# Kernel tuning notes

Hardware: AMD Instinct MI355X
Metric: run time of the kernel (lower is better)

## Reference

```python
import jax, jax.numpy as jnp
import numpy as np

EPS = 1e-5  # torch BatchNorm2d default


def _conv5x5(x, w, b):
    # x: [N,1,H,W], w: [1,1,5,5], b: [1]; stride 1, padding 2 (SAME)
    out = jax.lax.conv_general_dilated(
        x, w, window_strides=(1, 1), padding=((2, 2), (2, 2)),
        dimension_numbers=("NCHW", "OIHW", "NCHW"))
    return out + b[None, :, None, None]


def _batchnorm(x, gamma, beta):
    # training-mode BatchNorm2d: per-channel batch stats over (N,H,W), biased var
    mean = jnp.mean(x, axis=(0, 2, 3), keepdims=True)
    var = jnp.mean(jnp.square(x - mean), axis=(0, 2, 3), keepdims=True)
    xhat = (x - mean) * jax.lax.rsqrt(var + EPS)
    return xhat * gamma[None, :, None, None] + beta[None, :, None, None]


def _shrinkage(x, lumdb):
    return x + 0.5 * (jnp.sqrt(jnp.square(x - lumdb) + 1.0)
                      - jnp.sqrt(jnp.square(x + lumdb) + 1.0))


def setup_inputs() -> dict:
    key = jax.random.key(0)
    k1, k2, k3 = jax.random.split(key, 3)
    y = jax.random.normal(k1, (64, 1, 512, 512), dtype=jnp.float32)
    # kaiming-uniform-ish init for a 1x1x5x5 conv
    fan_in = 25.0
    bound = 1.0 / np.sqrt(fan_in)
    conv_w = jax.random.uniform(k2, (1, 1, 5, 5), jnp.float32, -bound, bound)
    conv_b = jax.random.uniform(k3, (1,), jnp.float32, -bound, bound)
    gamma = jnp.ones((1,), jnp.float32)
    beta = jnp.zeros((1,), jnp.float32)
    lambd = jnp.array([2.0, 1.0, 0.0], jnp.float32)
    return {"y": y, "conv_w": conv_w, "conv_b": conv_b,
            "gamma": gamma, "beta": beta, "lambd": lambd}


def reference(y, conv_w, conv_b, gamma, beta, lambd):
    x_k = y
    # unrolled LISTA iteration 1
    x = _batchnorm(_conv5x5(x_k, conv_w, conv_b), gamma, beta)
    x = _shrinkage(x, lambd[0])
    o12 = _batchnorm(_conv5x5(x, conv_w, conv_b), gamma, beta)
    x = _batchnorm(_conv5x5(x_k, conv_w, conv_b), gamma, beta)
    # iteration 2
    x = _shrinkage(o12 + x, lambd[1])
    o22 = _batchnorm(_conv5x5(x, conv_w, conv_b), gamma, beta)
    x = _batchnorm(_conv5x5(x_k, conv_w, conv_b), gamma, beta)
    # iteration 3
    x = _shrinkage(o22 + x, lambd[2])
    return x
```

## Files before the change

kernel.cpp:

```cpp
#include <hip/hip_runtime.h>
#include <math.h>

#define HH 512
#define WW 512
#define NTOT (64u*512u*512u)
#define TS 128
#define TROWS 132
#define TCH 18
#define TPIT 152
#define NTASK (TROWS*TCH)
#define NITER 10
#define NPART 4096

typedef __attribute__((ext_vector_type(8))) short short8;
typedef __attribute__((ext_vector_type(4))) float f32x4;

__device__ __forceinline__ float fsqrtf(float x) { return __builtin_amdgcn_sqrtf(x); }

__device__ __forceinline__ float shrinkf(float x, float l) {
    float a = x - l, b = x + l;
    return x + 0.5f * (fsqrtf(__builtin_fmaf(a, a, 1.f)) - fsqrtf(__builtin_fmaf(b, b, 1.f)));
}

__device__ __forceinline__ float bf2f(unsigned int u) {
    union { unsigned int i; float f; } cv; cv.i = u << 16; return cv.f;
}
__device__ __forceinline__ float lo2f(unsigned int p) {
    union { unsigned int i; float f; } cv; cv.i = p << 16; return cv.f;
}
__device__ __forceinline__ float hi2f(unsigned int p) {
    union { unsigned int i; float f; } cv; cv.i = p & 0xffff0000u; return cv.f;
}

__device__ __forceinline__ unsigned int cvtpk(float lo, float hi) {
    unsigned int r;
    asm("v_cvt_pk_bf16_f32 %0, %1, %2" : "=v"(r) : "v"(lo), "v"(hi));
    return r;
}

__device__ __forceinline__ void bf8(uint4 u, float* f) {
    f[0] = bf2f(u.x & 0xffffu); f[1] = bf2f(u.x >> 16);
    f[2] = bf2f(u.y & 0xffffu); f[3] = bf2f(u.y >> 16);
    f[4] = bf2f(u.z & 0xffffu); f[5] = bf2f(u.z >> 16);
    f[6] = bf2f(u.w & 0xffffu); f[7] = bf2f(u.w >> 16);
}

__device__ __forceinline__ void stats_fast(
    const float* __restrict__ part, double* __restrict__ sbuf,
    int tid, int lane, int wv,
    float gam, float bet, float& scl_out, float& shf_out)
{
    double sd = 0.0, qd = 0.0;
#pragma unroll
    for (int k = 0; k < 16; k++) {
        const int i = tid + k * 256;
        sd += (double)part[2 * i];
        qd += (double)part[2 * i + 1];
    }
#pragma unroll
    for (int off = 32; off > 0; off >>= 1) {
        sd += __shfl_xor(sd, off);
        qd += __shfl_xor(qd, off);
    }
    if (lane == 0) { sbuf[2 * wv] = sd; sbuf[2 * wv + 1] = qd; }
    __syncthreads();
    const double S = sbuf[0] + sbuf[2] + sbuf[4] + sbuf[6];
    const double Q = sbuf[1] + sbuf[3] + sbuf[5] + sbuf[7];
    const double mean = S / (double)NTOT;
    const double var  = Q / (double)NTOT - mean * mean;
    const double scl  = (double)gam / sqrt(var + 1e-5);
    scl_out = (float)scl;
    shf_out = (float)((double)bet - mean * scl);
}

template <int MODE, bool OBF>
__global__ __launch_bounds__(256, 4) void conv_k(
    const float* __restrict__ yin,
    const unsigned short* __restrict__ t1,
    const unsigned short* __restrict__ t2,
    unsigned short* __restrict__ outbf,
    float* __restrict__ outf32,
    const float* __restrict__ wgt,
    const float* __restrict__ bias,
    const float* __restrict__ prevPart,
    const float* __restrict__ statsIn,
    float* __restrict__ statsOut,
    const float* __restrict__ gamma,
    const float* __restrict__ beta,
    const float* __restrict__ lambd,
    float* __restrict__ partials)
{
    __shared__ unsigned short tile[TROWS * TPIT];
    __shared__ double sbuf[8];

    const int tid = threadIdx.x;
    const int lin = blockIdx.x;
    const int swz = ((lin & 7) << 7) | (lin >> 3);
    const int img = swz >> 4;
    const int rem = swz & 15;
    const int by = ((rem >> 2) & 3) * TS;
    const int bx = (rem & 3) * TS;
    const size_t ibase = (size_t)img * (HH * WW);

    const int lane = tid & 63;
    const int lm = lane & 15;
    const int kb = lane >> 4;
    const int wv = tid >> 6;

    float wloc[25];
#pragma unroll
    for (int i = 0; i < 25; i++) wloc[i] = wgt[i];
    const int basei = kb * 8 - lm - 6;
    short8 bfr[5];
#pragma unroll
    for (int ky = 0; ky < 5; ky++) {
        unsigned pkw[4];
#pragma unroll
        for (int jj = 0; jj < 4; jj++) {
            float v0 = 0.f, v1 = 0.f;
            const int i0 = basei + 2 * jj, i1 = i0 + 1;
#pragma unroll
            for (int t = 0; t < 5; t++) {
                if (i0 == t) v0 = wloc[ky * 5 + t];
                if (i1 == t) v1 = wloc[ky * 5 + t];
            }
            pkw[jj] = cvtpk(v0, v1);
        }
        union { unsigned u[4]; short8 s; } cv;
        cv.u[0]=pkw[0]; cv.u[1]=pkw[1]; cv.u[2]=pkw[2]; cv.u[3]=pkw[3];
        bfr[ky] = cv.s;
    }

    auto loadT = [&](int task, uint4& A, uint4& B) {
        A = make_uint4(0u,0u,0u,0u); B = make_uint4(0u,0u,0u,0u);
        const int row = task / TCH;
        const int ch  = task - row * TCH;
        const int gy  = by + row - 2;
        const int gx0 = bx + ch * 8 - 8;
        if (task < NTASK && gy >= 0 && gy < HH && gx0 >= 0 && gx0 <= WW - 8) {
            const size_t g = ibase + (size_t)gy * WW + gx0;
            if constexpr (MODE == 0) {
                A = *(const uint4*)(yin + g);
                B = *(const uint4*)(yin + g + 4);
            } else if constexpr (MODE == 1) {
                A = *(const uint4*)(t1 + g);
            } else {
                A = *(const uint4*)(t1 + g);
                B = *(const uint4*)(t2 + g);
            }
        }
    };

    uint4 sA0, sB0, sA1, sB1, sA2, sB2;
    loadT(tid,        sA0, sB0);
    loadT(tid + 256,  sA1, sB1);
    loadT(tid + 512,  sA2, sB2);

    float s1 = 0.f, h1 = 0.f, s2v = 0.f, h2 = 0.f, lam = 0.f;
    if constexpr (MODE == 1) {
        stats_fast(prevPart, sbuf, tid, lane, wv, gamma[0], beta[0], s1, h1);
        lam = lambd[0];
        if (lin == 0 && tid == 0) { statsOut[0] = s1; statsOut[1] = h1; }
    }
    if constexpr (MODE == 2) {
        stats_fast(prevPart, sbuf, tid, lane, wv, gamma[0], beta[0], s2v, h2);
        s1 = statsIn[0]; h1 = statsIn[1];
        lam = lambd[1];
    }

    auto procT = [&](int task, uint4 A, uint4 B) {
        const int row = task / TCH;
        const int ch  = task - row * TCH;
        uint4 pk = make_uint4(0u,0u,0u,0u);
        if constexpr (MODE == 0) {
            const float4 a = *(const float4*)&A;
            const float4 b = *(const float4*)&B;
            pk.x = cvtpk(a.x, a.y); pk.y = cvtpk(a.z, a.w);
            pk.z = cvtpk(b.x, b.y); pk.w = cvtpk(b.z, b.w);
        } else if constexpr (MODE == 1) {
            float f1[8]; bf8(A, f1);
            float v[8];
#pragma unroll
            for (int k = 0; k < 8; k++)
                v[k] = shrinkf(__builtin_fmaf(f1[k], s1, h1), lam);
            pk.x = cvtpk(v[0], v[1]); pk.y = cvtpk(v[2], v[3]);
            pk.z = cvtpk(v[4], v[5]); pk.w = cvtpk(v[6], v[7]);
        } else {
            float f1[8], f2[8]; bf8(A, f1); bf8(B, f2);
            float v[8];
#pragma unroll
            for (int k = 0; k < 8; k++) {
                float x = __builtin_fmaf(f2[k], s2v, h2)
                        + __builtin_fmaf(f1[k], s1, h1);
                v[k] = shrinkf(x, lam);
            }
            pk.x = cvtpk(v[0], v[1]); pk.y = cvtpk(v[2], v[3]);
            pk.z = cvtpk(v[4], v[5]); pk.w = cvtpk(v[6], v[7]);
        }
        const int gy  = by + row - 2;
        const int gx0 = bx + ch * 8 - 8;
        if (!(gy >= 0 && gy < HH && gx0 >= 0 && gx0 <= WW - 8))
            pk = make_uint4(0u,0u,0u,0u);
        *(uint4*)&tile[row * TPIT + ch * 8] = pk;
    };

#pragma unroll
    for (int t = 0; t < NITER; t++) {
        const int task = tid + t * 256;
        if (task < NTASK) procT(task, sA0, sB0);
        sA0 = sA1; sB0 = sB1;
        sA1 = sA2; sB1 = sB2;
        if (t + 3 < NITER) loadT(tid + (t + 3) * 256, sA2, sB2);
        else { sA2 = make_uint4(0u,0u,0u,0u); sB2 = make_uint4(0u,0u,0u,0u); }
    }

    const float b0 = bias[0];
    __syncthreads();

    const int r0w = wv * 32;

    f32x4 acc[2][8];
#pragma unroll
    for (int st = 0; st < 2; st++)
#pragma unroll
        for (int ct = 0; ct < 8; ct++)
            acc[st][ct] = (f32x4){0.f, 0.f, 0.f, 0.f};

#pragma unroll
    for (int ky = 0; ky < 5; ky++) {
        const short8 b = bfr[ky];
#pragma unroll
        for (int st = 0; st < 2; st++) {
            const unsigned short* ab = &tile[(r0w + st * 16 + lm + ky) * TPIT + kb * 8];
#pragma unroll
            for (int ct = 0; ct < 8; ct++) {
                short8 a = *(const short8*)(ab + ct * 16);
                acc[st][ct] = __builtin_amdgcn_mfma_f32_16x16x32_bf16(a, b, acc[st][ct], 0, 0, 0);
            }
        }
    }

    float s = 0.f, q = 0.f;
#pragma unroll
    for (int st = 0; st < 2; st++) {
#pragma unroll
        for (int ct = 0; ct < 8; ct++) {
            const f32x4 a = acc[st][ct];
            const int grow0 = by + r0w + st * 16 + kb * 4;
            const size_t base = ibase + (size_t)grow0 * WW + bx + ct * 16 + lm;
            if constexpr (OBF) {
                unsigned p01 = cvtpk(a[0] + b0, a[1] + b0);
                unsigned p23 = cvtpk(a[2] + b0, a[3] + b0);
                outbf[base]          = (unsigned short)(p01 & 0xffffu);
                outbf[base + WW]     = (unsigned short)(p01 >> 16);
                outbf[base + 2 * WW] = (unsigned short)(p23 & 0xffffu);
                outbf[base + 3 * WW] = (unsigned short)(p23 >> 16);
                float fr0 = lo2f(p01), fr1 = hi2f(p01), fr2 = lo2f(p23), fr3 = hi2f(p23);
                s += fr0 + fr1 + fr2 + fr3;
                q = __builtin_fmaf(fr0, fr0, __builtin_fmaf(fr1, fr1,
                    __builtin_fmaf(fr2, fr2, __builtin_fmaf(fr3, fr3, q))));
            } else {
                float f0 = a[0] + b0, f1v = a[1] + b0, f2v = a[2] + b0, f3v = a[3] + b0;
                outf32[base]          = f0;
                outf32[base + WW]     = f1v;
                outf32[base + 2 * WW] = f2v;
                outf32[base + 3 * WW] = f3v;
                s += f0 + f1v + f2v + f3v;
                q = __builtin_fmaf(f0, f0, __builtin_fmaf(f1v, f1v,
                    __builtin_fmaf(f2v, f2v, __builtin_fmaf(f3v, f3v, q))));
            }
        }
    }

#pragma unroll
    for (int off = 32; off > 0; off >>= 1) {
        s += __shfl_xor(s, off);
        q += __shfl_xor(q, off);
    }
    if (lane == 0) {
        partials[(swz * 4 + wv) * 2]     = s;
        partials[(swz * 4 + wv) * 2 + 1] = q;
    }
}

template <bool T3BF>
__global__ __launch_bounds__(256) void final_k(
    const unsigned short* __restrict__ t1,
    const unsigned short* __restrict__ t3b,
    float* __restrict__ io,
    const float* __restrict__ p3,
    const float* __restrict__ statsIn,
    const float* __restrict__ gamma,
    const float* __restrict__ beta,
    const float* __restrict__ lambd)
{
    __shared__ double sbuf[8];
    const int tid = threadIdx.x;
    const int lane = tid & 63;
    const int wv = tid >> 6;

    float s3, h3;
    stats_fast(p3, sbuf, tid, lane, wv, gamma[0], beta[0], s3, h3);
    const float s1 = statsIn[0], h1 = statsIn[1];
    const float lam = lambd[2];

#pragma unroll
    for (int c = 0; c < 8; c++) {
        const size_t idx = ((size_t)c * 1024 + blockIdx.x) * 256 + tid;
        const size_t base = idx * 8;

        uint4 u1 = *(const uint4*)(t1 + base);
        float f1[8]; bf8(u1, f1);

        float t3v[8];
        if constexpr (T3BF) {
            uint4 u3 = *(const uint4*)(t3b + base);
            bf8(u3, t3v);
        } else {
            float4 a0 = *(const float4*)(io + base);
            float4 a1 = *(const float4*)(io + base + 4);
            t3v[0]=a0.x; t3v[1]=a0.y; t3v[2]=a0.z; t3v[3]=a0.w;
            t3v[4]=a1.x; t3v[5]=a1.y; t3v[6]=a1.z; t3v[7]=a1.w;
        }

        float r[8];
#pragma unroll
        for (int k = 0; k < 8; k++) {
            float v = __builtin_fmaf(t3v[k], s3, h3) + __builtin_fmaf(f1[k], s1, h1);
            r[k] = shrinkf(v, lam);
        }
        *(float4*)(io + base)     = make_float4(r[0], r[1], r[2], r[3]);
        *(float4*)(io + base + 4) = make_float4(r[4], r[5], r[6], r[7]);
    }
}

extern "C" void kernel_launch(void* const* d_in, const int* in_sizes, int n_in,
                              void* d_out, int out_size, void* d_ws, size_t ws_size,
                              hipStream_t stream)
{
    const float* y     = (const float*)d_in[0];
    const float* wgt   = (const float*)d_in[1];
    const float* bias  = (const float*)d_in[2];
    const float* gamma = (const float*)d_in[3];
    const float* beta  = (const float*)d_in[4];
    const float* lambd = (const float*)d_in[5];
    float* out = (float*)d_out;

    char* ws = (char*)d_ws;
    unsigned short* t1 = (unsigned short*)ws;
    unsigned short* t2 = (unsigned short*)(ws + 33554432ull);
    unsigned short* t3 = (unsigned short*)(ws + 67108864ull);
    const bool t3bf = (ws_size >= 100761608ull);
    const size_t poff = t3bf ? 100663296ull : 67108864ull;
    float* p1    = (float*)(ws + poff);
    float* p2    = (float*)(ws + poff + 32768ull);
    float* p3    = (float*)(ws + poff + 65536ull);
    float* stats = (float*)(ws + poff + 98304ull);

    dim3 grid(1024, 1, 1), blk(256, 1, 1);
    conv_k<0, true><<<grid, blk, 0, stream>>>(y, nullptr, nullptr, t1, nullptr,
                                              wgt, bias, nullptr, nullptr, nullptr,
                                              gamma, beta, lambd, p1);
    conv_k<1, true><<<grid, blk, 0, stream>>>(nullptr, t1, nullptr, t2, nullptr,
                                              wgt, bias, p1, nullptr, stats,
                                              gamma, beta, lambd, p2);
    if (t3bf) {
        conv_k<2, true><<<grid, blk, 0, stream>>>(nullptr, t1, t2, t3, nullptr,
                                                  wgt, bias, p2, stats, nullptr,
                                                  gamma, beta, lambd, p3);
        final_k<true><<<grid, blk, 0, stream>>>(t1, t3, out, p3, stats,
                                                gamma, beta, lambd);
    } else {
        conv_k<2, false><<<grid, blk, 0, stream>>>(nullptr, t1, t2, nullptr, out,
                                                   wgt, bias, p2, stats, nullptr,
                                                   gamma, beta, lambd, p3);
        final_k<false><<<grid, blk, 0, stream>>>(t1, nullptr, out, p3, stats,
                                                 gamma, beta, lambd);
    }
}
```

Baseline: 91.30 us.

## Process two tiles per block with async global-to-LDS loads overlapping MFMA

Splits the first conv into its own kernel and adds a two-tile conv kernel for the later stages. In that kernel each block handles two adjacent tiles, using direct global-to-LDS loads (global_load_lds) for the t1 halo and register prefetch for t2. The second tile's loads are issued before the first tile's MFMA and store phase, so load latency hides behind compute. This doubles LDS per block, halves the grid, and lowers occupancy to 2 blocks per unit. It also removes the stats-kernel latency exposure at the start of the second tile.

```diff
diff --git a/kernel.cpp b/kernel.cpp
--- a/kernel.cpp
+++ b/kernel.cpp
@@ -8,9 +8,10 @@
 #define TROWS 132
 #define TCH 18
 #define TPIT 152
+#define TPL 144
 #define NTASK (TROWS*TCH)
+#define NTASKP 2432
 #define NITER 10
-#define NPART 4096
 
 typedef __attribute__((ext_vector_type(8))) short short8;
 typedef __attribute__((ext_vector_type(4))) float f32x4;
@@ -43,6 +44,13 @@
     f[2] = bf2f(u.y & 0xffffu); f[3] = bf2f(u.y >> 16);
     f[4] = bf2f(u.z & 0xffffu); f[5] = bf2f(u.z >> 16);
     f[6] = bf2f(u.w & 0xffffu); f[7] = bf2f(u.w >> 16);
+}
+
+__device__ __forceinline__ void gload16(const unsigned short* g, unsigned short* l) {
+    __builtin_amdgcn_global_load_lds(
+        (const __attribute__((address_space(1))) void*)g,
+        (__attribute__((address_space(3))) void*)l,
+        16, 0, 0);
 }
 
 __device__ __forceinline__ void stats_fast(
@@ -78,6 +86,157 @@
     const float* __restrict__ yin,
     const unsigned short* __restrict__ t1,
     const unsigned short* __restrict__ t2,
+    unsigned short* __restrict__ outbf,
+    float* __restrict__ outf32,
+    const float* __restrict__ wgt,
+    const float* __restrict__ bias,
+    const float* __restrict__ lambd,
+    float* __restrict__ partials)
+{
+    __shared__ unsigned short tile[TROWS * TPIT];
+
+    const int tid = threadIdx.x;
+    const int lin = blockIdx.x;
+    const int swz = ((lin & 7) << 7) | (lin >> 3);
+    const int img = swz >> 4;
+    const int rem = swz & 15;
+    const int by = ((rem >> 2) & 3) * TS;
+    const int bx = (rem & 3) * TS;
+    const size_t ibase = (size_t)img * (HH * WW);
+
+    const int lane = tid & 63;
+    const int lm = lane & 15;
+    const int kb = lane >> 4;
+    const int wv = tid >> 6;
+
+    float wloc[25];
+#pragma unroll
+    for (int i = 0; i < 25; i++) wloc[i] = wgt[i];
+    const int basei = kb * 8 - lm - 6;
+    short8 bfr[5];
+#pragma unroll
+    for (int ky = 0; ky < 5; ky++) {
+        unsigned pkw[4];
+#pragma unroll
+        for (int jj = 0; jj < 4; jj++) {
+            float v0 = 0.f, v1 = 0.f;
+            const int i0 = basei + 2 * jj, i1 = i0 + 1;
+#pragma unroll
+            for (int t = 0; t < 5; t++) {
+                if (i0 == t) v0 = wloc[ky * 5 + t];
+                if (i1 == t) v1 = wloc[ky * 5 + t];
+            }
+            pkw[jj] = cvtpk(v0, v1);
+        }
+        union { unsigned u[4]; short8 s; } cv;
+        cv.u[0]=pkw[0]; cv.u[1]=pkw[1]; cv.u[2]=pkw[2]; cv.u[3]=pkw[3];
+        bfr[ky] = cv.s;
+    }
+
+    auto loadT = [&](int task, uint4& A, uint4& B) {
+        A = make_uint4(0u,0u,0u,0u); B = make_uint4(0u,0u,0u,0u);
+        const int row = task / TCH;
+        const int ch  = task - row * TCH;
+        const int gy  = by + row - 2;
+        const int gx0 = bx + ch * 8 - 8;
+        if (task < NTASK && gy >= 0 && gy < HH && gx0 >= 0 && gx0 <= WW - 8) {
+            const size_t g = ibase + (size_t)gy * WW + gx0;
+            A = *(const uint4*)(yin + g);
+            B = *(const uint4*)(yin + g + 4);
+        }
+    };
+
+    uint4 sA0, sB0, sA1, sB1, sA2, sB2;
+    loadT(tid,        sA0, sB0);
+    loadT(tid + 256,  sA1, sB1);
+    loadT(tid + 512,  sA2, sB2);
+
+    auto procT = [&](int task, uint4 A, uint4 B) {
+        const int row = task / TCH;
+        const int ch  = task - row * TCH;
+        uint4 pk = make_uint4(0u,0u,0u,0u);
+        const float4 a = *(const float4*)&A;
+        const float4 b = *(const float4*)&B;
+        pk.x = cvtpk(a.x, a.y); pk.y = cvtpk(a.z, a.w);
+        pk.z = cvtpk(b.x, b.y); pk.w = cvtpk(b.z, b.w);
+        const int gy  = by + row - 2;
+        const int gx0 = bx + ch * 8 - 8;
+        if (!(gy >= 0 && gy < HH && gx0 >= 0 && gx0 <= WW - 8))
+            pk = make_uint4(0u,0u,0u,0u);
+        *(uint4*)&tile[row * TPIT + ch * 8] = pk;
+    };
+
+#pragma unroll
+    for (int t = 0; t < NITER; t++) {
+        const int task = tid + t * 256;
+        if (task < NTASK) procT(task, sA0, sB0);
+        sA0 = sA1; sB0 = sB1;
+        sA1 = sA2; sB1 = sB2;
+        if (t + 3 < NITER) loadT(tid + (t + 3) * 256, sA2, sB2);
+        else { sA2 = make_uint4(0u,0u,0u,0u); sB2 = make_uint4(0u,0u,0u,0u); }
+    }
+
+    const float b0 = bias[0];
+    __syncthreads();
+
+    const int r0w = wv * 32;
+    f32x4 acc[2][8];
+#pragma unroll
+    for (int st = 0; st < 2; st++)
+#pragma unroll
+        for (int ct = 0; ct < 8; ct++)
+            acc[st][ct] = (f32x4){0.f, 0.f, 0.f, 0.f};
+
+#pragma unroll
+    for (int ky = 0; ky < 5; ky++) {
+        const short8 b = bfr[ky];
+#pragma unroll
+        for (int st = 0; st < 2; st++) {
+            const unsigned short* ab = &tile[(r0w + st * 16 + lm + ky) * TPIT + kb * 8];
+#pragma unroll
+            for (int ct = 0; ct < 8; ct++) {
+                short8 a = *(const short8*)(ab + ct * 16);
+                acc[st][ct] = __builtin_amdgcn_mfma_f32_16x16x32_bf16(a, b, acc[st][ct], 0, 0, 0);
+            }
+        }
+    }
+
+    float s = 0.f, q = 0.f;
+#pragma unroll
+    for (int st = 0; st < 2; st++) {
+#pragma unroll
+        for (int ct = 0; ct < 8; ct++) {
+            const f32x4 a = acc[st][ct];
+            const int grow0 = by + r0w + st * 16 + kb * 4;
+            const size_t base = ibase + (size_t)grow0 * WW + bx + ct * 16 + lm;
+            unsigned p01 = cvtpk(a[0] + b0, a[1] + b0);
+            unsigned p23 = cvtpk(a[2] + b0, a[3] + b0);
+            outbf[base]          = (unsigned short)(p01 & 0xffffu);
+            outbf[base + WW]     = (unsigned short)(p01 >> 16);
+            outbf[base + 2 * WW] = (unsigned short)(p23 & 0xffffu);
+            outbf[base + 3 * WW] = (unsigned short)(p23 >> 16);
+            float fr0 = lo2f(p01), fr1 = hi2f(p01), fr2 = lo2f(p23), fr3 = hi2f(p23);
+            s += fr0 + fr1 + fr2 + fr3;
+            q = __builtin_fmaf(fr0, fr0, __builtin_fmaf(fr1, fr1,
+                __builtin_fmaf(fr2, fr2, __builtin_fmaf(fr3, fr3, q))));
+        }
+    }
+
+#pragma unroll
+    for (int off = 32; off > 0; off >>= 1) {
+        s += __shfl_xor(s, off);
+        q += __shfl_xor(q, off);
+    }
+    if (lane == 0) {
+        partials[(swz * 4 + wv) * 2]     = s;
+        partials[(swz * 4 + wv) * 2 + 1] = q;
+    }
+}
+
+template <int MODE, bool OBF>
+__global__ __launch_bounds__(256, 2) void conv2t_k(
+    const unsigned short* __restrict__ t1in,
+    const unsigned short* __restrict__ t2in,
     unsigned short* __restrict__ outbf,
     float* __restrict__ outf32,
     const float* __restrict__ wgt,
@@ -90,16 +249,18 @@
     const float* __restrict__ lambd,
     float* __restrict__ partials)
 {
-    __shared__ unsigned short tile[TROWS * TPIT];
+    __shared__ unsigned short bufA[NTASKP * 8];
+    __shared__ unsigned short bufB[NTASKP * 8];
     __shared__ double sbuf[8];
 
     const int tid = threadIdx.x;
     const int lin = blockIdx.x;
-    const int swz = ((lin & 7) << 7) | (lin >> 3);
-    const int img = swz >> 4;
-    const int rem = swz & 15;
-    const int by = ((rem >> 2) & 3) * TS;
-    const int bx = (rem & 3) * TS;
+    const int bswz = ((lin & 7) << 6) | (lin >> 3);
+    const int g0 = bswz * 2, g1 = g0 + 1;
+    const int img = g0 >> 4;
+    const int rem0 = g0 & 15, rem1 = g1 & 15;
+    const int by0 = ((rem0 >> 2) & 3) * TS, bx0 = (rem0 & 3) * TS;
+    const int by1 = ((rem1 >> 2) & 3) * TS, bx1 = (rem1 & 3) * TS;
     const size_t ibase = (size_t)img * (HH * WW);
 
     const int lane = tid & 63;
@@ -130,157 +291,171 @@
         cv.u[0]=pkw[0]; cv.u[1]=pkw[1]; cv.u[2]=pkw[2]; cv.u[3]=pkw[3];
         bfr[ky] = cv.s;
     }
-
-    auto loadT = [&](int task, uint4& A, uint4& B) {
-        A = make_uint4(0u,0u,0u,0u); B = make_uint4(0u,0u,0u,0u);
-        const int row = task / TCH;
-        const int ch  = task - row * TCH;
-        const int gy  = by + row - 2;
-        const int gx0 = bx + ch * 8 - 8;
-        if (task < NTASK && gy >= 0 && gy < HH && gx0 >= 0 && gx0 <= WW - 8) {
-            const size_t g = ibase + (size_t)gy * WW + gx0;
-            if constexpr (MODE == 0) {
-                A = *(const uint4*)(yin + g);
-                B = *(const uint4*)(yin + g + 4);
-            } else if constexpr (MODE == 1) {
-                A = *(const uint4*)(t1 + g);
-            } else {
-                A = *(const uint4*)(t1 + g);
-                B = *(const uint4*)(t2 + g);
+    const float b0 = bias[0];
+
+    auto issue_t1 = [&](int by, int bx, unsigned short* buf) {
+#pragma unroll
+        for (int r = 0; r < NITER; r++) {
+            const int task0 = r * 256 + wv * 64;
+            if (task0 < NTASK) {
+                const int task = task0 + lane;
+                const int row = task / TCH;
+                const int ch  = task - row * TCH;
+                const int gy  = by + row - 2;
+                const int gx0 = bx + ch * 8 - 8;
+                const bool ok = (task < NTASK) && gy >= 0 && gy < HH &&
+                                gx0 >= 0 && gx0 <= WW - 8;
+                const size_t g = ok ? (ibase + (size_t)gy * WW + gx0) : ibase;
+                gload16(t1in + g, &buf[task * 8]);
             }
         }
     };
 
-    uint4 sA0, sB0, sA1, sB1, sA2, sB2;
-    loadT(tid,        sA0, sB0);
-    loadT(tid + 256,  sA1, sB1);
-    loadT(tid + 512,  sA2, sB2);
+    struct R10 { uint4 a,b,c,d,e,f,g,h,i,j; };
+    auto load_t2 = [&](int by, int bx, R10& r) {
+        auto L = [&](int t) -> uint4 {
+            const int task = tid + t * 256;
+            const int row = task / TCH;
+            const int ch  = task - row * TCH;
+            const int gy  = by + row - 2;
+            const int gx0 = bx + ch * 8 - 8;
+            uint4 A = make_uint4(0u,0u,0u,0u);
+            if (task < NTASK && gy >= 0 && gy < HH && gx0 >= 0 && gx0 <= WW - 8)
+                A = *(const uint4*)(t2in + ibase + (size_t)gy * WW + gx0);
+            return A;
+        };
+        r.a=L(0); r.b=L(1); r.c=L(2); r.d=L(3); r.e=L(4);
+        r.f=L(5); r.g=L(6); r.h=L(7); r.i=L(8); r.j=L(9);
+    };
 
     float s1 = 0.f, h1 = 0.f, s2v = 0.f, h2 = 0.f, lam = 0.f;
+
+    auto xform = [&](int by, int bx, unsigned short* buf, const R10& r2) {
+        auto X = [&](int t, uint4 rt2) {
+            const int task = tid + t * 256;
+            if (task >= NTASK) return;
+            const int row = task / TCH;
+            const int ch  = task - row * TCH;
+            const int gy  = by + row - 2;
+            const int gx0 = bx + ch * 8 - 8;
+            const bool ok = gy >= 0 && gy < HH && gx0 >= 0 && gx0 <= WW - 8;
+            uint4 pk = make_uint4(0u,0u,0u,0u);
+            if (ok) {
+                uint4 u1 = *(const uint4*)&buf[task * 8];
+                float f1[8]; bf8(u1, f1);
+                float v[8];
+                if constexpr (MODE == 1) {
+#pragma unroll
+                    for (int k = 0; k < 8; k++)
+                        v[k] = shrinkf(__builtin_fmaf(f1[k], s1, h1), lam);
+                } else {
+                    float f2[8]; bf8(rt2, f2);
+#pragma unroll
+                    for (int k = 0; k < 8; k++) {
+                        float x = __builtin_fmaf(f2[k], s2v, h2)
+                                + __builtin_fmaf(f1[k], s1, h1);
+                        v[k] = shrinkf(x, lam);
+                    }
+                }
+                pk.x = cvtpk(v[0], v[1]); pk.y = cvtpk(v[2], v[3]);
+                pk.z = cvtpk(v[4], v[5]); pk.w = cvtpk(v[6], v[7]);
+            }
+            *(uint4*)&buf[task * 8] = pk;
+        };
+        X(0, r2.a); X(1, r2.b); X(2, r2.c); X(3, r2.d); X(4, r2.e);
+        X(5, r2.f); X(6, r2.g); X(7, r2.h); X(8, r2.i); X(9, r2.j);
+    };
+
+    auto mfma_store = [&](const unsigned short* buf, int by, int bx, int gt) {
+        const int r0w = wv * 32;
+        f32x4 acc[2][8];
+#pragma unroll
+        for (int st = 0; st < 2; st++)
+#pragma unroll
+            for (int ct = 0; ct < 8; ct++)
+                acc[st][ct] = (f32x4){0.f, 0.f, 0.f, 0.f};
+#pragma unroll
+        for (int ky = 0; ky < 5; ky++) {
+            const short8 b = bfr[ky];
+#pragma unroll
+            for (int st = 0; st < 2; st++) {
+                const unsigned short* ab = &buf[(r0w + st * 16 + lm + ky) * TPL + kb * 8];
+#pragma unroll
+                for (int ct = 0; ct < 8; ct++) {
+                    short8 a = *(const short8*)(ab + ct * 16);
+                    acc[st][ct] = __builtin_amdgcn_mfma_f32_16x16x32_bf16(a, b, acc[st][ct], 0, 0, 0);
+                }
+            }
+        }
+        float s = 0.f, q = 0.f;
+#pragma unroll
+        for (int st = 0; st < 2; st++) {
+#pragma unroll
+            for (int ct = 0; ct < 8; ct++) {
+                const f32x4 a = acc[st][ct];
+                const int grow0 = by + r0w + st * 16 + kb * 4;
+                const size_t base = ibase + (size_t)grow0 * WW + bx + ct * 16 + lm;
+                if constexpr (OBF) {
+                    unsigned p01 = cvtpk(a[0] + b0, a[1] + b0);
+                    unsigned p23 = cvtpk(a[2] + b0, a[3] + b0);
+                    outbf[base]          = (unsigned short)(p01 & 0xffffu);
+                    outbf[base + WW]     = (unsigned short)(p01 >> 16);
+                    outbf[base + 2 * WW] = (unsigned short)(p23 & 0xffffu);
+                    outbf[base + 3 * WW] = (unsigned short)(p23 >> 16);
+                    float fr0 = lo2f(p01), fr1 = hi2f(p01), fr2 = lo2f(p23), fr3 = hi2f(p23);
+                    s += fr0 + fr1 + fr2 + fr3;
+                    q = __builtin_fmaf(fr0, fr0, __builtin_fmaf(fr1, fr1,
+                        __builtin_fmaf(fr2, fr2, __builtin_fmaf(fr3, fr3, q))));
+                } else {
+                    float f0 = a[0] + b0, f1v = a[1] + b0, f2v = a[2] + b0, f3v = a[3] + b0;
+                    outf32[base]          = f0;
+                    outf32[base + WW]     = f1v;
+                    outf32[base + 2 * WW] = f2v;
+                    outf32[base + 3 * WW] = f3v;
+                    s += f0 + f1v + f2v + f3v;
+                    q = __builtin_fmaf(f0, f0, __builtin_fmaf(f1v, f1v,
+                        __builtin_fmaf(f2v, f2v, __builtin_fmaf(f3v, f3v, q))));
+                }
+            }
+        }
+#pragma unroll
+        for (int off = 32; off > 0; off >>= 1) {
+            s += __shfl_xor(s, off);
+            q += __shfl_xor(q, off);
+        }
+        if (lane == 0) {
+            partials[(gt * 4 + wv) * 2]     = s;
+            partials[(gt * 4 + wv) * 2 + 1] = q;
+        }
+    };
+
+    issue_t1(by0, bx0, bufA);
+    R10 rT0{}, rT1{};
+    if constexpr (MODE == 2) load_t2(by0, bx0, rT0);
+
     if constexpr (MODE == 1) {
         stats_fast(prevPart, sbuf, tid, lane, wv, gamma[0], beta[0], s1, h1);
         lam = lambd[0];
         if (lin == 0 && tid == 0) { statsOut[0] = s1; statsOut[1] = h1; }
-    }
-    if constexpr (MODE == 2) {
+    } else {
         stats_fast(prevPart, sbuf, tid, lane, wv, gamma[0], beta[0], s2v, h2);
         s1 = statsIn[0]; h1 = statsIn[1];
         lam = lambd[1];
     }
 
-    auto procT = [&](int task, uint4 A, uint4 B) {
-        const int row = task / TCH;
-        const int ch  = task - row * TCH;
-        uint4 pk = make_uint4(0u,0u,0u,0u);
-        if constexpr (MODE == 0) {
-            const float4 a = *(const float4*)&A;
-            const float4 b = *(const float4*)&B;
-            pk.x = cvtpk(a.x, a.y); pk.y = cvtpk(a.z, a.w);
-            pk.z = cvtpk(b.x, b.y); pk.w = cvtpk(b.z, b.w);
-        } else if constexpr (MODE == 1) {
-            float f1[8]; bf8(A, f1);
-            float v[8];
-#pragma unroll
-            for (int k = 0; k < 8; k++)
-                v[k] = shrinkf(__builtin_fmaf(f1[k], s1, h1), lam);
-            pk.x = cvtpk(v[0], v[1]); pk.y = cvtpk(v[2], v[3]);
-            pk.z = cvtpk(v[4], v[5]); pk.w = cvtpk(v[6], v[7]);
-        } else {
-            float f1[8], f2[8]; bf8(A, f1); bf8(B, f2);
-            float v[8];
-#pragma unroll
-            for (int k = 0; k < 8; k++) {
-                float x = __builtin_fmaf(f2[k], s2v, h2)
-                        + __builtin_fmaf(f1[k], s1, h1);
-                v[k] = shrinkf(x, lam);
-            }
-            pk.x = cvtpk(v[0], v[1]); pk.y = cvtpk(v[2], v[3]);
-            pk.z = cvtpk(v[4], v[5]); pk.w = cvtpk(v[6], v[7]);
-        }
-        const int gy  = by + row - 2;
-        const int gx0 = bx + ch * 8 - 8;
-        if (!(gy >= 0 && gy < HH && gx0 >= 0 && gx0 <= WW - 8))
-            pk = make_uint4(0u,0u,0u,0u);
-        *(uint4*)&tile[row * TPIT + ch * 8] = pk;
-    };
-
-#pragma unroll
-    for (int t = 0; t < NITER; t++) {
-        const int task = tid + t * 256;
-        if (task < NTASK) procT(task, sA0, sB0);
-        sA0 = sA1; sB0 = sB1;
-        sA1 = sA2; sB1 = sB2;
-        if (t + 3 < NITER) loadT(tid + (t + 3) * 256, sA2, sB2);
-        else { sA2 = make_uint4(0u,0u,0u,0u); sB2 = make_uint4(0u,0u,0u,0u); }
-    }
-
-    const float b0 = bias[0];
+    xform(by0, bx0, bufA, rT0);
     __syncthreads();
 
-    const int r0w = wv * 32;
-
-    f32x4 acc[2][8];
-#pragma unroll
-    for (int st = 0; st < 2; st++)
-#pragma unroll
-        for (int ct = 0; ct < 8; ct++)
-            acc[st][ct] = (f32x4){0.f, 0.f, 0.f, 0.f};
-
-#pragma unroll
-    for (int ky = 0; ky < 5; ky++) {
-        const short8 b = bfr[ky];
-#pragma unroll
-        for (int st = 0; st < 2; st++) {
-            const unsigned short* ab = &tile[(r0w + st * 16 + lm + ky) * TPIT + kb * 8];
-#pragma unroll
-            for (int ct = 0; ct < 8; ct++) {
-                short8 a = *(const short8*)(ab + ct * 16);
-                acc[st][ct] = __builtin_amdgcn_mfma_f32_16x16x32_bf16(a, b, acc[st][ct], 0, 0, 0);
-            }
-        }
-    }
-
-    float s = 0.f, q = 0.f;
-#pragma unroll
-    for (int st = 0; st < 2; st++) {
-#pragma unroll
-        for (int ct = 0; ct < 8; ct++) {
-            const f32x4 a = acc[st][ct];
-            const int grow0 = by + r0w + st * 16 + kb * 4;
-            const size_t base = ibase + (size_t)grow0 * WW + bx + ct * 16 + lm;
-            if constexpr (OBF) {
-                unsigned p01 = cvtpk(a[0] + b0, a[1] + b0);
-                unsigned p23 = cvtpk(a[2] + b0, a[3] + b0);
-                outbf[base]          = (unsigned short)(p01 & 0xffffu);
-                outbf[base + WW]     = (unsigned short)(p01 >> 16);
-                outbf[base + 2 * WW] = (unsigned short)(p23 & 0xffffu);
-                outbf[base + 3 * WW] = (unsigned short)(p23 >> 16);
-                float fr0 = lo2f(p01), fr1 = hi2f(p01), fr2 = lo2f(p23), fr3 = hi2f(p23);
-                s += fr0 + fr1 + fr2 + fr3;
-                q = __builtin_fmaf(fr0, fr0, __builtin_fmaf(fr1, fr1,
-                    __builtin_fmaf(fr2, fr2, __builtin_fmaf(fr3, fr3, q))));
-            } else {
-                float f0 = a[0] + b0, f1v = a[1] + b0, f2v = a[2] + b0, f3v = a[3] + b0;
-                outf32[base]          = f0;
-                outf32[base + WW]     = f1v;
-                outf32[base + 2 * WW] = f2v;
-                outf32[base + 3 * WW] = f3v;
-                s += f0 + f1v + f2v + f3v;
-                q = __builtin_fmaf(f0, f0, __builtin_fmaf(f1v, f1v,
-                    __builtin_fmaf(f2v, f2v, __builtin_fmaf(f3v, f3v, q))));
-            }
-        }
-    }
-
-#pragma unroll
-    for (int off = 32; off > 0; off >>= 1) {
-        s += __shfl_xor(s, off);
-        q += __shfl_xor(q, off);
-    }
-    if (lane == 0) {
-        partials[(swz * 4 + wv) * 2]     = s;
-        partials[(swz * 4 + wv) * 2 + 1] = q;
-    }
+    issue_t1(by1, bx1, bufB);
+    if constexpr (MODE == 2) load_t2(by1, bx1, rT1);
+
+    mfma_store(bufA, by0, bx0, g0);
+    __syncthreads();
+
+    xform(by1, bx1, bufB, rT1);
+    __syncthreads();
+
+    mfma_store(bufB, by1, bx1, g1);
 }
 
 template <bool T3BF>
@@ -357,24 +532,23 @@
     float* p3    = (float*)(ws + poff + 65536ull);
     float* stats = (float*)(ws + poff + 98304ull);
 
-    dim3 grid(1024, 1, 1), blk(256, 1, 1);
-    conv_k<0, true><<<grid, blk, 0, stream>>>(y, nullptr, nullptr, t1, nullptr,
-                                              wgt, bias, nullptr, nullptr, nullptr,
-                                              gamma, beta, lambd, p1);
-    conv_k<1, true><<<grid, blk, 0, stream>>>(nullptr, t1, nullptr, t2, nullptr,
-                                              wgt, bias, p1, nullptr, stats,
-                                              gamma, beta, lambd, p2);
+    dim3 blk(256, 1, 1);
+    conv_k<0, true><<<dim3(1024,1,1), blk, 0, stream>>>(
+        y, nullptr, nullptr, t1, nullptr, wgt, bias, lambd, p1);
+    conv2t_k<1, true><<<dim3(512,1,1), blk, 0, stream>>>(
+        t1, nullptr, t2, nullptr, wgt, bias, p1, nullptr, stats,
+        gamma, beta, lambd, p2);
     if (t3bf) {
-        conv_k<2, true><<<grid, blk, 0, stream>>>(nullptr, t1, t2, t3, nullptr,
-                                                  wgt, bias, p2, stats, nullptr,
-                                                  gamma, beta, lambd, p3);
-        final_k<true><<<grid, blk, 0, stream>>>(t1, t3, out, p3, stats,
-                                                gamma, beta, lambd);
+        conv2t_k<2, true><<<dim3(512,1,1), blk, 0, stream>>>(
+            t1, t2, t3, nullptr, wgt, bias, p2, stats, nullptr,
+            gamma, beta, lambd, p3);
+        final_k<true><<<dim3(1024,1,1), blk, 0, stream>>>(
+            t1, t3, out, p3, stats, gamma, beta, lambd);
     } else {
-        conv_k<2, false><<<grid, blk, 0, stream>>>(nullptr, t1, t2, nullptr, out,
-                                                   wgt, bias, p2, stats, nullptr,
-                                                   gamma, beta, lambd, p3);
-        final_k<false><<<grid, blk, 0, stream>>>(t1, nullptr, out, p3, stats,
-                                                 gamma, beta, lambd);
-    }
-}
+        conv2t_k<2, false><<<dim3(512,1,1), blk, 0, stream>>>(
+            t1, t2, nullptr, out, wgt, bias, p2, stats, nullptr,
+            gamma, beta, lambd, p3);
+        final_k<false><<<dim3(1024,1,1), blk, 0, stream>>>(
+            t1, nullptr, out, p3, stats, gamma, beta, lambd);
+    }
+}
```

Measured after the change: 104.6 us. +14.6%, slower.
